# Kernel tuning notes

Hardware: AMD Instinct MI355X
Metric: run time of the kernel (lower is better)

## Reference

```python
import jax, jax.numpy as jnp
import numpy as np

N_NODES = 100000
N_EDGES = 3200000
DIM = 16


def setup_inputs() -> dict:
    key = jax.random.key(0)
    k1, k2, k3, k4 = jax.random.split(key, 4)
    state_input = jax.random.normal(k1, (N_NODES, DIM), dtype=jnp.float32)
    row = jax.random.randint(k2, (N_EDGES,), 0, N_NODES, dtype=jnp.int32)
    col = jax.random.randint(k3, (N_EDGES,), 0, N_NODES, dtype=jnp.int32)
    edge_weights = jax.random.uniform(k4, (N_EDGES,), dtype=jnp.float32)
    return {"state_input": state_input, "row": row, "col": col,
            "edge_weights": edge_weights}


def reference(state_input, row, col, edge_weights):
    # f_eq: per-dim self dynamics, f(x) = -x  -> [N, dim]
    self_diff = -state_input

    # gather pair endpoints: x_1 = state[col], x_2 = state[row]
    # g_eq: sin(x_2 - x_1) per dim (Kuramoto-style coupling) -> [E, dim]
    neighbor_processed = jnp.sin(state_input[row] - state_input[col])

    # weight by edge weight and scatter-sum into destination nodes (col)
    aggregated_sum = jax.ops.segment_sum(
        neighbor_processed * edge_weights[:, None], col,
        num_segments=state_input.shape[0])  # [N, dim]

    # s_eq: elementwise tanh on aggregated sum
    interact_diff = jnp.tanh(aggregated_sum)

    return (self_diff + interact_diff,
            (state_input, self_diff),
            (aggregated_sum, interact_diff))
```

## Files before the change

kernel.cpp:

```cpp
#include <hip/hip_runtime.h>
#include <hip/hip_fp16.h>
#include <math.h>

#define N_NODES 100000
#define N_EDGES 3200000
#define DIM 16
#define NSZ (N_NODES * DIM)

#define NPB 128
#define NBUCK 782
#define NBLK 512
#define EPB 6250
#define CAP 4864
#define PRK 10

typedef float nvec4 __attribute__((ext_vector_type(4)));

__global__ __launch_bounds__(512)
void hist_table(const float* __restrict__ state, __half* __restrict__ hs,
                const int* __restrict__ col, unsigned* __restrict__ tbl) {
    __shared__ int hcnt[NBUCK];
    int t = threadIdx.x, blk = blockIdx.x;
    for (int j = t; j < NBUCK; j += 512) hcnt[j] = 0;
    for (int i = blk * 512 + t; i < NSZ / 4; i += NBLK * 512) {
        nvec4 v = __builtin_nontemporal_load(&((const nvec4*)state)[i]);
        union { __half2 h[2]; float2 f; } u;
        u.h[0] = __floats2half2_rn(v.x, v.y);
        u.h[1] = __floats2half2_rn(v.z, v.w);
        ((float2*)hs)[i] = u.f;
    }
    __syncthreads();
    int e0 = blk * EPB;
    for (int i = t; i < EPB; i += 512)
        atomicAdd(&hcnt[col[e0 + i] >> 7], 1);
    __syncthreads();
    for (int j = t; j < NBUCK; j += 512)
        tbl[(size_t)j * NBLK + blk] = (unsigned)hcnt[j];
}

__global__ __launch_bounds__(256)
void col_reduce(const unsigned* __restrict__ tbl, int* __restrict__ totals) {
    __shared__ int s[256];
    int b = blockIdx.x, t = threadIdx.x;
    int v = (int)tbl[(size_t)b * NBLK + t] + (int)tbl[(size_t)b * NBLK + 256 + t];
    s[t] = v;
    __syncthreads();
    for (int d = 128; d > 0; d >>= 1) {
        if (t < d) s[t] += s[t + d];
        __syncthreads();
    }
    if (t == 0) totals[b] = s[0];
}

__global__ __launch_bounds__(1024)
void scan_off(const int* __restrict__ totals, int* __restrict__ off) {
    __shared__ int s[1024];
    int t = threadIdx.x;
    int v = (t < NBUCK) ? totals[t] : 0;
    s[t] = v;
    __syncthreads();
    for (int d = 1; d < 1024; d <<= 1) {
        int u = (t >= d) ? s[t - d] : 0;
        __syncthreads();
        s[t] += u;
        __syncthreads();
    }
    if (t < NBUCK) off[t + 1] = s[t];
    if (t == 0) off[0] = 0;
}

__global__ __launch_bounds__(512)
void base_scan(unsigned* __restrict__ tbl, const int* __restrict__ off) {
    __shared__ int s[512];
    int b = blockIdx.x, t = threadIdx.x;
    int v = (int)tbl[(size_t)b * NBLK + t];
    s[t] = v;
    __syncthreads();
    for (int d = 1; d < 512; d <<= 1) {
        int u = (t >= d) ? s[t - d] : 0;
        __syncthreads();
        s[t] += u;
        __syncthreads();
    }
    tbl[(size_t)b * NBLK + t] = (unsigned)(off[b] + s[t] - v);
}

__global__ __launch_bounds__(512)
void sort_write(const int* __restrict__ row, const int* __restrict__ col,
                const float* __restrict__ w, const unsigned* __restrict__ tbl,
                const int* __restrict__ off,
                unsigned long long* __restrict__ packed) {
    __shared__ unsigned long long sbuf[EPB];
    __shared__ int sc[1024];
    __shared__ int cur[NBUCK];
    __shared__ int gbase[NBUCK];
    int t = threadIdx.x, blk = blockIdx.x;
    int e0 = blk * EPB;

    for (int j = t; j < NBUCK; j += 512) {
        int b0 = (int)tbl[(size_t)j * NBLK + blk];
        int b1 = (blk == NBLK - 1) ? off[j + 1]
                                   : (int)tbl[(size_t)j * NBLK + blk + 1];
        gbase[j] = b0;
        cur[j] = b1 - b0;
    }
    __syncthreads();
    sc[t]       = (t < NBUCK)       ? cur[t]       : 0;
    sc[t + 512] = (t + 512 < NBUCK) ? cur[t + 512] : 0;
    __syncthreads();
    for (int d = 1; d < 1024; d <<= 1) {
        int u1 = (t >= d) ? sc[t - d] : 0;
        int u2 = sc[t + 512 - d];
        __syncthreads();
        sc[t] += u1;
        sc[t + 512] += u2;
        __syncthreads();
    }
    for (int j = t; j < NBUCK; j += 512) {
        int ex = sc[j] - cur[j];
        sc[j] = ex;
        cur[j] = ex;
    }
    __syncthreads();
    for (int i = t; i < EPB; i += 512) {
        int e = e0 + i;
        int c = col[e];
        int pos = atomicAdd(&cur[c >> 7], 1);
        sbuf[pos] = ((unsigned long long)(unsigned)c << 47)
                  | ((unsigned long long)(unsigned)row[e] << 30)
                  | (unsigned long long)(__float_as_uint(w[e]) >> 2);
    }
    __syncthreads();
    for (int i = t; i < EPB; i += 512) {
        unsigned long long pv = sbuf[i];
        int b = (int)(pv >> 54);
        __builtin_nontemporal_store(pv, &packed[gbase[b] + (i - sc[b])]);
    }
}

__device__ inline float4 edge_acc(float4 a, const float4 xx,
                                  unsigned long long p, float2 hbits) {
    union { float2 f; __half2 h[2]; } u; u.f = hbits;
    float2 lo = __half22float2(u.h[0]);
    float2 hi = __half22float2(u.h[1]);
    float we = __uint_as_float(((unsigned)p & 0x3FFFFFFFu) << 2);
    a.x += __sinf(lo.x - xx.x) * we;
    a.y += __sinf(lo.y - xx.y) * we;
    a.z += __sinf(hi.x - xx.z) * we;
    a.w += __sinf(hi.y - xx.w) * we;
    return a;
}

__global__ __launch_bounds__(512)
void bucket_sort_aggregate(const float* __restrict__ state,
                           const __half2* __restrict__ hs2,
                           const int* __restrict__ off,
                           const unsigned long long* __restrict__ packed,
                           float* __restrict__ out) {
    __shared__ unsigned long long sbuf[CAP];
    __shared__ int s_cnt[NPB], s_start[NPB], s_cur[NPB];
    int b = blockIdx.x, t = threadIdx.x;
    int g = t >> 2, q = t & 3;
    int beg = off[b], end = off[b + 1];

    int n = b * NPB + g;
    bool valid = (n < N_NODES);
    float4 xx = valid ? ((const float4*)state)[n * 4 + q]
                      : make_float4(0.f, 0.f, 0.f, 0.f);
    float4 acc = make_float4(0.f, 0.f, 0.f, 0.f);
    const float2* hsf2 = (const float2*)hs2;

    for (int tbeg = beg; tbeg < end; tbeg += CAP) {
        int tend = tbeg + CAP; if (tend > end) tend = end;
        if (t < NPB) s_cnt[t] = 0;
        __syncthreads();

        unsigned long long pr[PRK];
        #pragma unroll
        for (int k = 0; k < PRK; ++k) {
            int e = tbeg + t + k * 512;
            if (e < tend) {
                pr[k] = __builtin_nontemporal_load(&packed[e]);
                atomicAdd(&s_cnt[(unsigned)(pr[k] >> 47) & 127u], 1);
            }
        }
        __syncthreads();

        if (t < NPB) s_start[t] = s_cnt[t];
        __syncthreads();
        for (int d = 1; d < NPB; d <<= 1) {
            int u = 0;
            if (t < NPB && t >= d) u = s_start[t - d];
            __syncthreads();
            if (t < NPB) s_start[t] += u;
            __syncthreads();
        }
        if (t < NPB) {
            int ex = s_start[t] - s_cnt[t];
            s_start[t] = ex;
            s_cur[t] = ex;
        }
        __syncthreads();

        #pragma unroll
        for (int k = 0; k < PRK; ++k) {
            int e = tbeg + t + k * 512;
            if (e < tend) {
                int cl = (int)((pr[k] >> 47) & 127u);
                int pos = atomicAdd(&s_cur[cl], 1);
                sbuf[pos] = pr[k];
            }
        }
        __syncthreads();

        {
            int es = s_start[g], ee = s_cur[g];
            float4 a = acc;
            int e = es;
            for (; e + 4 <= ee; e += 4) {
                unsigned long long p0 = sbuf[e + 0];
                unsigned long long p1 = sbuf[e + 1];
                unsigned long long p2 = sbuf[e + 2];
                unsigned long long p3 = sbuf[e + 3];
                float2 h0 = hsf2[(unsigned)((p0 >> 30) & 0x1FFFFu) * 4u + q];
                float2 h1 = hsf2[(unsigned)((p1 >> 30) & 0x1FFFFu) * 4u + q];
                float2 h2 = hsf2[(unsigned)((p2 >> 30) & 0x1FFFFu) * 4u + q];
                float2 h3 = hsf2[(unsigned)((p3 >> 30) & 0x1FFFFu) * 4u + q];
                a = edge_acc(a, xx, p0, h0);
                a = edge_acc(a, xx, p1, h1);
                a = edge_acc(a, xx, p2, h2);
                a = edge_acc(a, xx, p3, h3);
            }
            for (; e < ee; ++e) {
                unsigned long long p0 = sbuf[e];
                float2 h0 = hsf2[(unsigned)((p0 >> 30) & 0x1FFFFu) * 4u + q];
                a = edge_acc(a, xx, p0, h0);
            }
            acc = a;
        }
        __syncthreads();
    }

    if (valid) {
        float4 th = make_float4(tanhf(acc.x), tanhf(acc.y),
                                tanhf(acc.z), tanhf(acc.w));
        int gdx = n * 4 + q;
        ((float4*)(out + 0 * (size_t)NSZ))[gdx] =
            make_float4(th.x - xx.x, th.y - xx.y, th.z - xx.z, th.w - xx.w);
        ((float4*)(out + 1 * (size_t)NSZ))[gdx] = xx;
        ((float4*)(out + 2 * (size_t)NSZ))[gdx] =
            make_float4(-xx.x, -xx.y, -xx.z, -xx.w);
        ((float4*)(out + 3 * (size_t)NSZ))[gdx] = acc;
        ((float4*)(out + 4 * (size_t)NSZ))[gdx] = th;
    }
}

__global__ __launch_bounds__(256)
void edge_kernel(const float* __restrict__ state, const int* __restrict__ row,
                 const int* __restrict__ col, const float* __restrict__ w,
                 float* __restrict__ agg) {
    int idx = blockIdx.x * blockDim.x + threadIdx.x;
    if (idx >= N_EDGES * 4) return;
    int e = idx >> 2, qq = idx & 3;
    int r = row[e], c = col[e];
    float we = w[e];
    const float4 xr = ((const float4*)state)[r * 4 + qq];
    const float4 xcv = ((const float4*)state)[c * 4 + qq];
    float* dst = agg + c * DIM + qq * 4;
    atomicAdd(dst + 0, sinf(xr.x - xcv.x) * we);
    atomicAdd(dst + 1, sinf(xr.y - xcv.y) * we);
    atomicAdd(dst + 2, sinf(xr.z - xcv.z) * we);
    atomicAdd(dst + 3, sinf(xr.w - xcv.w) * we);
}

__global__ __launch_bounds__(256)
void node_kernel(const float* __restrict__ state, const float* __restrict__ agg,
                 float* __restrict__ out) {
    int idx = blockIdx.x * blockDim.x + threadIdx.x;
    if (idx >= N_NODES * 4) return;
    float4 x = ((const float4*)state)[idx];
    float4 a = ((const float4*)agg)[idx];
    float4 tv = make_float4(tanhf(a.x), tanhf(a.y), tanhf(a.z), tanhf(a.w));
    ((float4*)(out + 0 * NSZ))[idx] = make_float4(tv.x - x.x, tv.y - x.y,
                                                  tv.z - x.z, tv.w - x.w);
    ((float4*)(out + 1 * NSZ))[idx] = x;
    ((float4*)(out + 2 * NSZ))[idx] = make_float4(-x.x, -x.y, -x.z, -x.w);
    ((float4*)(out + 4 * NSZ))[idx] = tv;
}

extern "C" void kernel_launch(void* const* d_in, const int* in_sizes, int n_in,
                              void* d_out, int out_size, void* d_ws, size_t ws_size,
                              hipStream_t stream) {
    const float* state = (const float*)d_in[0];
    const int*   row   = (const int*)d_in[1];
    const int*   col   = (const int*)d_in[2];
    const float* w     = (const float*)d_in[3];
    float* out = (float*)d_out;

    size_t packed_off = 0;
    size_t half_off   = packed_off + (size_t)N_EDGES * 8;
    size_t tbl_off    = half_off + (size_t)NSZ * 2;
    size_t tot_off    = tbl_off + (size_t)NBUCK * NBLK * 4;
    size_t off_off    = tot_off + (size_t)NBUCK * 4;
    size_t needed     = off_off + (size_t)(NBUCK + 1) * 4;

    if (ws_size >= needed) {
        unsigned long long* packed =
            (unsigned long long*)((char*)d_ws + packed_off);
        __half* hs    = (__half*)((char*)d_ws + half_off);
        unsigned* tbl = (unsigned*)((char*)d_ws + tbl_off);
        int* totals   = (int*)((char*)d_ws + tot_off);
        int* off      = (int*)((char*)d_ws + off_off);

        hist_table<<<NBLK, 512, 0, stream>>>(state, hs, col, tbl);
        col_reduce<<<NBUCK, 256, 0, stream>>>(tbl, totals);
        scan_off<<<1, 1024, 0, stream>>>(totals, off);
        base_scan<<<NBUCK, 512, 0, stream>>>(tbl, off);
        sort_write<<<NBLK, 512, 0, stream>>>(row, col, w, tbl, off, packed);
        bucket_sort_aggregate<<<NBUCK, 512, 0, stream>>>(
            state, (const __half2*)hs, off, packed, out);
    } else {
        float* agg = out + 3 * NSZ;
        (void)hipMemsetAsync(agg, 0, NSZ * sizeof(float), stream);
        edge_kernel<<<(N_EDGES * 4 + 255) / 256, 256, 0, stream>>>(
            state, row, col, w, agg);
        node_kernel<<<(N_NODES * 4 + 255) / 256, 256, 0, stream>>>(
            state, agg, out);
    }
}
```

Measured before the change: 181.9 us.

## Fuse bucket totals into histogram, use wave-shuffle scans, split edges per node

Removes the col_reduce kernel by having hist_table atomically add per-bucket totals, with a memset to zero them first. The LDS Hillis-Steele scans in scan_off, base_scan, sort_write and the aggregate kernel become wave-level shuffle scans. Column, row and weight loads are vectorized to int4/float4, using EPB 6256 so each block's edge range is a multiple of 4. The aggregate kernel runs 1024 threads with two threads per node quarter, each taking alternate edges and combining via shuffle, and the output stores are split between the two. This aims to cut launches and barriers and raise per-node parallelism, at the cost of extra global atomics and shuffle work.

```diff
diff --git a/kernel.cpp b/kernel.cpp
--- a/kernel.cpp
+++ b/kernel.cpp
@@ -10,15 +10,16 @@
 #define NPB 128
 #define NBUCK 782
 #define NBLK 512
-#define EPB 6250
+#define EPB 6256
 #define CAP 4864
-#define PRK 10
+#define PRK 5
 
 typedef float nvec4 __attribute__((ext_vector_type(4)));
 
 __global__ __launch_bounds__(512)
 void hist_table(const float* __restrict__ state, __half* __restrict__ hs,
-                const int* __restrict__ col, unsigned* __restrict__ tbl) {
+                const int* __restrict__ col, unsigned* __restrict__ tbl,
+                int* __restrict__ totals) {
     __shared__ int hcnt[NBUCK];
     int t = threadIdx.x, blk = blockIdx.x;
     for (int j = t; j < NBUCK; j += 512) hcnt[j] = 0;
@@ -31,58 +32,65 @@
     }
     __syncthreads();
     int e0 = blk * EPB;
-    for (int i = t; i < EPB; i += 512)
-        atomicAdd(&hcnt[col[e0 + i] >> 7], 1);
-    __syncthreads();
-    for (int j = t; j < NBUCK; j += 512)
-        tbl[(size_t)j * NBLK + blk] = (unsigned)hcnt[j];
-}
-
-__global__ __launch_bounds__(256)
-void col_reduce(const unsigned* __restrict__ tbl, int* __restrict__ totals) {
-    __shared__ int s[256];
-    int b = blockIdx.x, t = threadIdx.x;
-    int v = (int)tbl[(size_t)b * NBLK + t] + (int)tbl[(size_t)b * NBLK + 256 + t];
-    s[t] = v;
-    __syncthreads();
-    for (int d = 128; d > 0; d >>= 1) {
-        if (t < d) s[t] += s[t + d];
-        __syncthreads();
-    }
-    if (t == 0) totals[b] = s[0];
+    int eN = e0 + EPB; if (eN > N_EDGES) eN = N_EDGES;
+    int nch = (eN - e0) >> 2;
+    const int4* c4p = (const int4*)(col + e0);
+    for (int i = t; i < nch; i += 512) {
+        int4 c = c4p[i];
+        atomicAdd(&hcnt[c.x >> 7], 1);
+        atomicAdd(&hcnt[c.y >> 7], 1);
+        atomicAdd(&hcnt[c.z >> 7], 1);
+        atomicAdd(&hcnt[c.w >> 7], 1);
+    }
+    __syncthreads();
+    for (int j = t; j < NBUCK; j += 512) {
+        int c = hcnt[j];
+        tbl[(size_t)j * NBLK + blk] = (unsigned)c;
+        if (c) atomicAdd(&totals[j], c);
+    }
 }
 
 __global__ __launch_bounds__(1024)
 void scan_off(const int* __restrict__ totals, int* __restrict__ off) {
-    __shared__ int s[1024];
+    __shared__ int wsum[16];
     int t = threadIdx.x;
-    int v = (t < NBUCK) ? totals[t] : 0;
-    s[t] = v;
-    __syncthreads();
-    for (int d = 1; d < 1024; d <<= 1) {
-        int u = (t >= d) ? s[t - d] : 0;
-        __syncthreads();
-        s[t] += u;
-        __syncthreads();
-    }
-    if (t < NBUCK) off[t + 1] = s[t];
+    int i0 = 2 * t, i1 = 2 * t + 1;
+    int v0 = (i0 < NBUCK) ? totals[i0] : 0;
+    int v1 = (i1 < NBUCK) ? totals[i1] : 0;
+    int p = v0 + v1, ps = p;
+    #pragma unroll
+    for (int d = 1; d < 64; d <<= 1) {
+        int u = __shfl_up(ps, d, 64);
+        if ((t & 63) >= d) ps += u;
+    }
+    if ((t & 63) == 63) wsum[t >> 6] = ps;
+    __syncthreads();
+    int wid = t >> 6, wbase = 0;
+    #pragma unroll
+    for (int k = 0; k < 16; ++k) wbase += (k < wid) ? wsum[k] : 0;
+    int ex = wbase + ps - p;
+    if (i0 < NBUCK) off[i0 + 1] = ex + v0;
+    if (i1 < NBUCK) off[i1 + 1] = ex + v0 + v1;
     if (t == 0) off[0] = 0;
 }
 
 __global__ __launch_bounds__(512)
 void base_scan(unsigned* __restrict__ tbl, const int* __restrict__ off) {
-    __shared__ int s[512];
+    __shared__ int wsum[8];
     int b = blockIdx.x, t = threadIdx.x;
     int v = (int)tbl[(size_t)b * NBLK + t];
-    s[t] = v;
-    __syncthreads();
-    for (int d = 1; d < 512; d <<= 1) {
-        int u = (t >= d) ? s[t - d] : 0;
-        __syncthreads();
-        s[t] += u;
-        __syncthreads();
-    }
-    tbl[(size_t)b * NBLK + t] = (unsigned)(off[b] + s[t] - v);
+    int ps = v;
+    #pragma unroll
+    for (int d = 1; d < 64; d <<= 1) {
+        int u = __shfl_up(ps, d, 64);
+        if ((t & 63) >= d) ps += u;
+    }
+    if ((t & 63) == 63) wsum[t >> 6] = ps;
+    __syncthreads();
+    int wid = t >> 6, wbase = 0;
+    #pragma unroll
+    for (int k = 0; k < 8; ++k) wbase += (k < wid) ? wsum[k] : 0;
+    tbl[(size_t)b * NBLK + t] = (unsigned)(off[b] + wbase + ps - v);
 }
 
 __global__ __launch_bounds__(512)
@@ -94,8 +102,11 @@
     __shared__ int sc[1024];
     __shared__ int cur[NBUCK];
     __shared__ int gbase[NBUCK];
+    __shared__ int wsum[8];
     int t = threadIdx.x, blk = blockIdx.x;
     int e0 = blk * EPB;
+    int eN = e0 + EPB; if (eN > N_EDGES) eN = N_EDGES;
+    int cnt = eN - e0;
 
     for (int j = t; j < NBUCK; j += 512) {
         int b0 = (int)tbl[(size_t)j * NBLK + blk];
@@ -105,33 +116,54 @@
         cur[j] = b1 - b0;
     }
     __syncthreads();
-    sc[t]       = (t < NBUCK)       ? cur[t]       : 0;
-    sc[t + 512] = (t + 512 < NBUCK) ? cur[t + 512] : 0;
-    __syncthreads();
-    for (int d = 1; d < 1024; d <<= 1) {
-        int u1 = (t >= d) ? sc[t - d] : 0;
-        int u2 = sc[t + 512 - d];
-        __syncthreads();
-        sc[t] += u1;
-        sc[t + 512] += u2;
-        __syncthreads();
-    }
-    for (int j = t; j < NBUCK; j += 512) {
-        int ex = sc[j] - cur[j];
-        sc[j] = ex;
-        cur[j] = ex;
-    }
-    __syncthreads();
-    for (int i = t; i < EPB; i += 512) {
-        int e = e0 + i;
-        int c = col[e];
-        int pos = atomicAdd(&cur[c >> 7], 1);
-        sbuf[pos] = ((unsigned long long)(unsigned)c << 47)
-                  | ((unsigned long long)(unsigned)row[e] << 30)
-                  | (unsigned long long)(__float_as_uint(w[e]) >> 2);
-    }
-    __syncthreads();
-    for (int i = t; i < EPB; i += 512) {
+    {
+        int i0 = 2 * t, i1 = 2 * t + 1;
+        int v0 = (i0 < NBUCK) ? cur[i0] : 0;
+        int v1 = (i1 < NBUCK) ? cur[i1] : 0;
+        int p = v0 + v1, ps = p;
+        #pragma unroll
+        for (int d = 1; d < 64; d <<= 1) {
+            int u = __shfl_up(ps, d, 64);
+            if ((t & 63) >= d) ps += u;
+        }
+        if ((t & 63) == 63) wsum[t >> 6] = ps;
+        __syncthreads();
+        int wid = t >> 6, wbase = 0;
+        #pragma unroll
+        for (int k = 0; k < 8; ++k) wbase += (k < wid) ? wsum[k] : 0;
+        int ex = wbase + ps - p;
+        if (i0 < NBUCK) { sc[i0] = ex;      cur[i0] = ex; }
+        if (i1 < NBUCK) { sc[i1] = ex + v0; cur[i1] = ex + v0; }
+    }
+    __syncthreads();
+    {
+        int nch = cnt >> 2;
+        const int4*  c4p = (const int4*)(col + e0);
+        const int4*  r4p = (const int4*)(row + e0);
+        const float4* w4p = (const float4*)(w + e0);
+        for (int i = t; i < nch; i += 512) {
+            int4 c = c4p[i]; int4 r = r4p[i]; float4 ww = w4p[i];
+            int pos;
+            pos = atomicAdd(&cur[c.x >> 7], 1);
+            sbuf[pos] = ((unsigned long long)(unsigned)c.x << 47)
+                      | ((unsigned long long)(unsigned)r.x << 30)
+                      | (unsigned long long)(__float_as_uint(ww.x) >> 2);
+            pos = atomicAdd(&cur[c.y >> 7], 1);
+            sbuf[pos] = ((unsigned long long)(unsigned)c.y << 47)
+                      | ((unsigned long long)(unsigned)r.y << 30)
+                      | (unsigned long long)(__float_as_uint(ww.y) >> 2);
+            pos = atomicAdd(&cur[c.z >> 7], 1);
+            sbuf[pos] = ((unsigned long long)(unsigned)c.z << 47)
+                      | ((unsigned long long)(unsigned)r.z << 30)
+                      | (unsigned long long)(__float_as_uint(ww.z) >> 2);
+            pos = atomicAdd(&cur[c.w >> 7], 1);
+            sbuf[pos] = ((unsigned long long)(unsigned)c.w << 47)
+                      | ((unsigned long long)(unsigned)r.w << 30)
+                      | (unsigned long long)(__float_as_uint(ww.w) >> 2);
+        }
+    }
+    __syncthreads();
+    for (int i = t; i < cnt; i += 512) {
         unsigned long long pv = sbuf[i];
         int b = (int)(pv >> 54);
         __builtin_nontemporal_store(pv, &packed[gbase[b] + (i - sc[b])]);
@@ -151,7 +183,7 @@
     return a;
 }
 
-__global__ __launch_bounds__(512)
+__global__ __launch_bounds__(1024, 8)
 void bucket_sort_aggregate(const float* __restrict__ state,
                            const __half2* __restrict__ hs2,
                            const int* __restrict__ off,
@@ -159,8 +191,9 @@
                            float* __restrict__ out) {
     __shared__ unsigned long long sbuf[CAP];
     __shared__ int s_cnt[NPB], s_start[NPB], s_cur[NPB];
+    __shared__ int s_wsum;
     int b = blockIdx.x, t = threadIdx.x;
-    int g = t >> 2, q = t & 3;
+    int q = t & 3, sub = (t >> 2) & 1, g = t >> 3;
     int beg = off[b], end = off[b + 1];
 
     int n = b * NPB + g;
@@ -178,7 +211,7 @@
         unsigned long long pr[PRK];
         #pragma unroll
         for (int k = 0; k < PRK; ++k) {
-            int e = tbeg + t + k * 512;
+            int e = tbeg + t + k * 1024;
             if (e < tend) {
                 pr[k] = __builtin_nontemporal_load(&packed[e]);
                 atomicAdd(&s_cnt[(unsigned)(pr[k] >> 47) & 127u], 1);
@@ -186,25 +219,27 @@
         }
         __syncthreads();
 
-        if (t < NPB) s_start[t] = s_cnt[t];
-        __syncthreads();
-        for (int d = 1; d < NPB; d <<= 1) {
-            int u = 0;
-            if (t < NPB && t >= d) u = s_start[t - d];
+        {
+            int v = (t < NPB) ? s_cnt[t] : 0;
+            int ps = v;
+            #pragma unroll
+            for (int d = 1; d < 64; d <<= 1) {
+                int u = __shfl_up(ps, d, 64);
+                if ((t & 63) >= d) ps += u;
+            }
+            if (t == 63) s_wsum = ps;
             __syncthreads();
-            if (t < NPB) s_start[t] += u;
-            __syncthreads();
-        }
-        if (t < NPB) {
-            int ex = s_start[t] - s_cnt[t];
-            s_start[t] = ex;
-            s_cur[t] = ex;
+            if (t < NPB) {
+                int ex = ps - v + ((t >= 64) ? s_wsum : 0);
+                s_start[t] = ex;
+                s_cur[t] = ex;
+            }
         }
         __syncthreads();
 
         #pragma unroll
         for (int k = 0; k < PRK; ++k) {
-            int e = tbeg + t + k * 512;
+            int e = tbeg + t + k * 1024;
             if (e < tend) {
                 int cl = (int)((pr[k] >> 47) & 127u);
                 int pos = atomicAdd(&s_cur[cl], 1);
@@ -216,12 +251,12 @@
         {
             int es = s_start[g], ee = s_cur[g];
             float4 a = acc;
-            int e = es;
-            for (; e + 4 <= ee; e += 4) {
-                unsigned long long p0 = sbuf[e + 0];
-                unsigned long long p1 = sbuf[e + 1];
-                unsigned long long p2 = sbuf[e + 2];
-                unsigned long long p3 = sbuf[e + 3];
+            int e = es + sub;
+            for (; e + 6 < ee; e += 8) {
+                unsigned long long p0 = sbuf[e];
+                unsigned long long p1 = sbuf[e + 2];
+                unsigned long long p2 = sbuf[e + 4];
+                unsigned long long p3 = sbuf[e + 6];
                 float2 h0 = hsf2[(unsigned)((p0 >> 30) & 0x1FFFFu) * 4u + q];
                 float2 h1 = hsf2[(unsigned)((p1 >> 30) & 0x1FFFFu) * 4u + q];
                 float2 h2 = hsf2[(unsigned)((p2 >> 30) & 0x1FFFFu) * 4u + q];
@@ -231,7 +266,7 @@
                 a = edge_acc(a, xx, p2, h2);
                 a = edge_acc(a, xx, p3, h3);
             }
-            for (; e < ee; ++e) {
+            for (; e < ee; e += 2) {
                 unsigned long long p0 = sbuf[e];
                 float2 h0 = hsf2[(unsigned)((p0 >> 30) & 0x1FFFFu) * 4u + q];
                 a = edge_acc(a, xx, p0, h0);
@@ -240,18 +275,26 @@
         }
         __syncthreads();
     }
+
+    acc.x += __shfl_xor(acc.x, 4, 64);
+    acc.y += __shfl_xor(acc.y, 4, 64);
+    acc.z += __shfl_xor(acc.z, 4, 64);
+    acc.w += __shfl_xor(acc.w, 4, 64);
 
     if (valid) {
         float4 th = make_float4(tanhf(acc.x), tanhf(acc.y),
                                 tanhf(acc.z), tanhf(acc.w));
         int gdx = n * 4 + q;
-        ((float4*)(out + 0 * (size_t)NSZ))[gdx] =
-            make_float4(th.x - xx.x, th.y - xx.y, th.z - xx.z, th.w - xx.w);
-        ((float4*)(out + 1 * (size_t)NSZ))[gdx] = xx;
-        ((float4*)(out + 2 * (size_t)NSZ))[gdx] =
-            make_float4(-xx.x, -xx.y, -xx.z, -xx.w);
-        ((float4*)(out + 3 * (size_t)NSZ))[gdx] = acc;
-        ((float4*)(out + 4 * (size_t)NSZ))[gdx] = th;
+        if (sub == 0) {
+            ((float4*)(out + 0 * (size_t)NSZ))[gdx] =
+                make_float4(th.x - xx.x, th.y - xx.y, th.z - xx.z, th.w - xx.w);
+            ((float4*)(out + 2 * (size_t)NSZ))[gdx] =
+                make_float4(-xx.x, -xx.y, -xx.z, -xx.w);
+            ((float4*)(out + 4 * (size_t)NSZ))[gdx] = th;
+        } else {
+            ((float4*)(out + 1 * (size_t)NSZ))[gdx] = xx;
+            ((float4*)(out + 3 * (size_t)NSZ))[gdx] = acc;
+        }
     }
 }
 
@@ -312,12 +355,12 @@
         int* totals   = (int*)((char*)d_ws + tot_off);
         int* off      = (int*)((char*)d_ws + off_off);
 
-        hist_table<<<NBLK, 512, 0, stream>>>(state, hs, col, tbl);
-        col_reduce<<<NBUCK, 256, 0, stream>>>(tbl, totals);
+        (void)hipMemsetAsync(totals, 0, (size_t)NBUCK * sizeof(int), stream);
+        hist_table<<<NBLK, 512, 0, stream>>>(state, hs, col, tbl, totals);
         scan_off<<<1, 1024, 0, stream>>>(totals, off);
         base_scan<<<NBUCK, 512, 0, stream>>>(tbl, off);
         sort_write<<<NBLK, 512, 0, stream>>>(row, col, w, tbl, off, packed);
-        bucket_sort_aggregate<<<NBUCK, 512, 0, stream>>>(
+        bucket_sort_aggregate<<<NBUCK, 1024, 0, stream>>>(
             state, (const __half2*)hs, off, packed, out);
     } else {
         float* agg = out + 3 * NSZ;
```

Result: no change. 185.5 us (+1.9%).
